# Kernel optimization log

Measured on AMD Instinct MI355X. Metric: run time of the kernel, lower is better.

## Reference

```python
import jax, jax.numpy as jnp
import numpy as np

N = 50000   # nodes
E = 800000  # directed edges
D = 128     # input_channels


def _kaiming(key, shape):
    fan_in = shape[0]
    return jax.random.normal(key, shape, jnp.float32) * np.float32(np.sqrt(2.0 / fan_in))


def setup_inputs():
    key = jax.random.key(0)
    ks = jax.random.split(key, 8)
    x = jax.random.normal(ks[0], (N, D), jnp.float32)
    edge_index = jax.random.randint(ks[1], (2, E), 0, N, dtype=jnp.int32)
    return {
        "x": x,
        "edge_index": edge_index,
        "W_in": _kaiming(ks[2], (D, D)),      "b_in": jnp.zeros((D,), jnp.float32),
        "W1": _kaiming(ks[3], (D, 2 * D)),    "b1": jnp.zeros((2 * D,), jnp.float32),
        "W2": _kaiming(ks[4], (2 * D, D)),    "b2": jnp.zeros((D,), jnp.float32),
        "W3": _kaiming(ks[5], (D, D // 2)),   "b3": jnp.zeros((D // 2,), jnp.float32),
        "W_out": _kaiming(ks[6], (D // 2, 1)), "b_out": jnp.zeros((1,), jnp.float32),
    }


def _gcn_conv(x, src, dst, W, b, n):
    """PyG GCNConv: add self-loops, symmetric D^-1/2 (A+I) D^-1/2 normalization."""
    h = x @ W  # [n, out]
    loop = jnp.arange(n, dtype=src.dtype)
    s = jnp.concatenate([src, loop])  # message sources (x_j)
    d = jnp.concatenate([dst, loop])  # aggregation targets (x_i)
    deg = jax.ops.segment_sum(jnp.ones_like(d, jnp.float32), d, num_segments=n)
    dis = jnp.where(deg > 0, jax.lax.rsqrt(jnp.maximum(deg, 1.0)), 0.0)
    norm = dis[s] * dis[d]  # [E+n]
    msg = h[s] * norm[:, None]  # gather + scale
    out = jax.ops.segment_sum(msg, d, num_segments=n)  # scatter-add
    return out + b


def reference(x, edge_index, W_in, b_in, W1, b1, W2, b2, W3, b3, W_out, b_out):
    src, dst = edge_index[0], edge_index[1]
    n = x.shape[0]
    lrelu = lambda t: jax.nn.leaky_relu(t, 0.01)
    # dropout in eval mode (identity)
    h = lrelu(x @ W_in + b_in)
    h = lrelu(_gcn_conv(h, src, dst, W1, b1, n))
    h = lrelu(_gcn_conv(h, src, dst, W2, b2, n))
    h = lrelu(_gcn_conv(h, src, dst, W3, b3, n))
    return h @ W_out + b_out  # [n, 1]
```

## Files before the change

### kernel.cpp

```cpp
#include <hip/hip_runtime.h>
#include <hip/hip_cooperative_groups.h>

namespace cg = cooperative_groups;


#define LRELU(v) ((v) > 0.f ? (v) : 0.01f * (v))

typedef __attribute__((ext_vector_type(8))) _Float16 half8;
typedef __attribute__((ext_vector_type(8))) float float8;
typedef __attribute__((ext_vector_type(4))) float floatx4;

constexpr int CAP = 64;
constexpr int SMEM_H = 16896;

template <int K, int F, int EPI, typename IT>
__device__ void phase_gemm(const IT* __restrict__ X,
                           const _Float16* __restrict__ Wt,
                           const float* __restrict__ b,
                           const int* __restrict__ cnt,
                           _Float16* __restrict__ out, int M,
                           _Float16* xs) {
  constexpr int TM = 64;
  constexpr int LK = K + 8;
  constexpr int CW = F / 4;
  constexpr int NT = CW / 16;
  constexpr int NK = K / 32;

  const int tid = threadIdx.x;
  const int w = tid >> 6;
  const int lane = tid & 63;
  const int m = lane & 15;
  const int q = lane >> 4;
  const int nTiles = (M + TM - 1) / TM;

  half8 breg[NT][NK];
#pragma unroll
  for (int t = 0; t < NT; ++t)
#pragma unroll
    for (int kc = 0; kc < NK; ++kc)
      breg[t][kc] =
          *(const half8*)&Wt[(long)(w * CW + t * 16 + m) * K + kc * 32 + q * 8];

  for (int tile = blockIdx.x; tile < nTiles; tile += gridDim.x) {
    const int m0 = tile * TM;
    __syncthreads();
    constexpr int CPR = K / 8;
    for (int idx = tid; idx < TM * CPR; idx += 256) {
      const int row = idx / CPR;
      const int kk = idx % CPR;
      const int g = m0 + row;
      half8 h = (half8)(_Float16)0.f;
      if (g < M) {
        if constexpr (sizeof(IT) == 4) {
          const float4* p = (const float4*)&X[(long)g * K + kk * 8];
          float4 a = p[0], c = p[1];
          h[0] = (_Float16)a.x; h[1] = (_Float16)a.y;
          h[2] = (_Float16)a.z; h[3] = (_Float16)a.w;
          h[4] = (_Float16)c.x; h[5] = (_Float16)c.y;
          h[6] = (_Float16)c.z; h[7] = (_Float16)c.w;
        } else {
          h = *(const half8*)&X[(long)g * K + kk * 8];
        }
      }
      *(half8*)&xs[row * LK + kk * 8] = h;
    }
    __syncthreads();

    floatx4 acc[4][NT];
#pragma unroll
    for (int rt = 0; rt < 4; ++rt)
#pragma unroll
      for (int t = 0; t < NT; ++t) acc[rt][t] = (floatx4){0.f, 0.f, 0.f, 0.f};

#pragma unroll
    for (int kc = 0; kc < NK; ++kc) {
      half8 af[4];
#pragma unroll
      for (int rt = 0; rt < 4; ++rt)
        af[rt] = *(const half8*)&xs[(rt * 16 + m) * LK + kc * 32 + q * 8];
#pragma unroll
      for (int rt = 0; rt < 4; ++rt)
#pragma unroll
        for (int t = 0; t < NT; ++t)
          acc[rt][t] = __builtin_amdgcn_mfma_f32_16x16x32_f16(
              af[rt], breg[t][kc], acc[rt][t], 0, 0, 0);
    }

#pragma unroll
    for (int rt = 0; rt < 4; ++rt) {
#pragma unroll
      for (int r = 0; r < 4; ++r) {
        const int row = m0 + rt * 16 + q * 4 + r;
        if (row < M) {
          const float dv = rsqrtf((float)cnt[row] + 1.0f);
#pragma unroll
          for (int t = 0; t < NT; ++t) {
            const int col = w * CW + t * 16 + m;
            float v = acc[rt][t][r];
            if constexpr (EPI == 0) { v += b[col]; v = LRELU(v); v *= dv; }
            if constexpr (EPI == 2) { v *= dv; }
            out[(long)row * F + col] = (_Float16)v;
          }
        }
      }
    }
  }
}

__device__ void phase_gemm2x(const _Float16* __restrict__ X,
                             const _Float16* __restrict__ Wt1,
                             const float* __restrict__ b1,
                             const _Float16* __restrict__ Wt2,
                             const int* __restrict__ cnt,
                             _Float16* __restrict__ out, int M,
                             _Float16* smem) {
  constexpr int TM = 64;
  constexpr int LK1 = 128 + 8;
  constexpr int LK2 = 256 + 8;
  _Float16* xs = smem;
  _Float16* ys = smem;

  const int tid = threadIdx.x;
  const int w = tid >> 6;
  const int lane = tid & 63;
  const int m = lane & 15;
  const int q = lane >> 4;
  const int nTiles = (M + TM - 1) / TM;

  half8 breg1[4][4];
#pragma unroll
  for (int t = 0; t < 4; ++t)
#pragma unroll
    for (int kc = 0; kc < 4; ++kc)
      breg1[t][kc] = *(const half8*)&Wt1[(long)(w * 64 + t * 16 + m) * 128 +
                                         kc * 32 + q * 8];
  half8 breg2[2][8];
#pragma unroll
  for (int t = 0; t < 2; ++t)
#pragma unroll
    for (int kc = 0; kc < 8; ++kc)
      breg2[t][kc] = *(const half8*)&Wt2[(long)(w * 32 + t * 16 + m) * 256 +
                                         kc * 32 + q * 8];

  for (int tile = blockIdx.x; tile < nTiles; tile += gridDim.x) {
    const int m0 = tile * TM;
    __syncthreads();
    for (int idx = tid; idx < TM * 16; idx += 256) {
      const int row = idx >> 4;
      const int kk = idx & 15;
      const int g = m0 + row;
      half8 h = (half8)(_Float16)0.f;
      if (g < M) h = *(const half8*)&X[(long)g * 128 + kk * 8];
      *(half8*)&xs[row * LK1 + kk * 8] = h;
    }
    __syncthreads();

    floatx4 acc1[4][4];
#pragma unroll
    for (int rt = 0; rt < 4; ++rt)
#pragma unroll
      for (int t = 0; t < 4; ++t) acc1[rt][t] = (floatx4){0.f, 0.f, 0.f, 0.f};

#pragma unroll
    for (int kc = 0; kc < 4; ++kc) {
      half8 af[4];
#pragma unroll
      for (int rt = 0; rt < 4; ++rt)
        af[rt] = *(const half8*)&xs[(rt * 16 + m) * LK1 + kc * 32 + q * 8];
#pragma unroll
      for (int rt = 0; rt < 4; ++rt)
#pragma unroll
        for (int t = 0; t < 4; ++t)
          acc1[rt][t] = __builtin_amdgcn_mfma_f32_16x16x32_f16(
              af[rt], breg1[t][kc], acc1[rt][t], 0, 0, 0);
    }
    __syncthreads();

#pragma unroll
    for (int rt = 0; rt < 4; ++rt) {
#pragma unroll
      for (int r = 0; r < 4; ++r) {
        const int row = rt * 16 + q * 4 + r;
#pragma unroll
        for (int t = 0; t < 4; ++t) {
          const int col = w * 64 + t * 16 + m;
          float v = acc1[rt][t][r] + b1[col];
          ys[row * LK2 + col] = (_Float16)LRELU(v);
        }
      }
    }
    __syncthreads();

    floatx4 acc2[4][2];
#pragma unroll
    for (int rt = 0; rt < 4; ++rt)
#pragma unroll
      for (int t = 0; t < 2; ++t) acc2[rt][t] = (floatx4){0.f, 0.f, 0.f, 0.f};

#pragma unroll
    for (int kc = 0; kc < 8; ++kc) {
      half8 af[4];
#pragma unroll
      for (int rt = 0; rt < 4; ++rt)
        af[rt] = *(const half8*)&ys[(rt * 16 + m) * LK2 + kc * 32 + q * 8];
#pragma unroll
      for (int rt = 0; rt < 4; ++rt)
#pragma unroll
        for (int t = 0; t < 2; ++t)
          acc2[rt][t] = __builtin_amdgcn_mfma_f32_16x16x32_f16(
              af[rt], breg2[t][kc], acc2[rt][t], 0, 0, 0);
    }

#pragma unroll
    for (int rt = 0; rt < 4; ++rt) {
#pragma unroll
      for (int r = 0; r < 4; ++r) {
        const int row = m0 + rt * 16 + q * 4 + r;
        if (row < M) {
          const float dv = rsqrtf((float)cnt[row] + 1.0f);
#pragma unroll
          for (int t = 0; t < 2; ++t) {
            const int col = w * 32 + t * 16 + m;
            out[(long)row * 128 + col] = (_Float16)(acc2[rt][t][r] * dv);
          }
        }
      }
    }
  }
}

template <int F, int MODE>
__device__ void phase_agg(const _Float16* __restrict__ G,
                          const unsigned short* __restrict__ pad,
                          const int* __restrict__ cnt,
                          const float* __restrict__ b,
                          const float* __restrict__ Wout,
                          const float* __restrict__ bout,
                          void* __restrict__ out, int N) {
  const int w = threadIdx.x >> 6;
  const int lane = threadIdx.x & 63;
  const int c = lane & 7;
  const int j = lane >> 3;
  const int n = j >> 2;
  const int jj = j & 3;
  const int uBlk = (N + 7) / 8;
  const int nUnits = (F == 128) ? 2 * uBlk : uBlk;

  for (int u = blockIdx.x; u < nUnits; u += gridDim.x) {
    const int y = (F == 128) ? (u / uBlk) : 0;
    const int ub = (F == 128) ? (u % uBlk) : u;
    int i = ub * 8 + w * 2 + n;
    const bool valid = (i < N);
    if (!valid) i = N - 1;
    const int col0 = y << 6;

    const _Float16* gbase = G + col0 + c * 8;
    const int cn = min(cnt[i], CAP);
    const unsigned short* plist = pad + (long)i * CAP;

    float8 acc = {0.f, 0.f, 0.f, 0.f, 0.f, 0.f, 0.f, 0.f};
    if (jj == 0)
      acc = __builtin_convertvector(*(const half8*)(gbase + (long)i * F), float8);
    for (int e = jj; e < cn; e += 4) {
      const int s = plist[e];
      acc += __builtin_convertvector(*(const half8*)(gbase + (long)s * F), float8);
    }
#pragma unroll
    for (int k = 0; k < 8; ++k) {
      acc[k] += __shfl_xor(acc[k], 8);
      acc[k] += __shfl_xor(acc[k], 16);
    }

    const float dv = rsqrtf((float)cnt[i] + 1.0f);
    if constexpr (MODE == 2) {
      float p = 0.f;
#pragma unroll
      for (int k = 0; k < 8; ++k) {
        const int col = c * 8 + k;
        float v = acc[k] * dv + b[col];
        v = LRELU(v);
        p += v * Wout[col];
      }
      p += __shfl_xor(p, 1);
      p += __shfl_xor(p, 2);
      p += __shfl_xor(p, 4);
      if (valid && jj == 0 && c == 0) ((float*)out)[i] = p + bout[0];
    } else {
      if (valid && jj == 0) {
        half8 hv;
#pragma unroll
        for (int k = 0; k < 8; ++k) {
          float v = acc[k] * dv;
          if constexpr (MODE == 1) { v += b[col0 + c * 8 + k]; v = LRELU(v); }
          hv[k] = (_Float16)v;
        }
        *(half8*)&((_Float16*)out)[(long)i * F + col0 + c * 8] = hv;
      }
    }
  }
}

__global__ __launch_bounds__(256, 2) void k_mega(
    const float* __restrict__ x, const int* __restrict__ src,
    const int* __restrict__ dst, const float* __restrict__ W_in,
    const float* __restrict__ b_in, const float* __restrict__ W1,
    const float* __restrict__ b1, const float* __restrict__ W2,
    const float* __restrict__ b2, const float* __restrict__ W3,
    const float* __restrict__ b3, const float* __restrict__ W_out,
    const float* __restrict__ b_out, int* __restrict__ cnt,
    unsigned short* __restrict__ pad, _Float16* __restrict__ wt_in,
    _Float16* __restrict__ wt1, _Float16* __restrict__ wt2,
    _Float16* __restrict__ wt3, _Float16* __restrict__ buf1,
    _Float16* __restrict__ buf2, _Float16* __restrict__ buf3,
    float* __restrict__ out, int N, int E, int PR) {
  cg::grid_group grid = cg::this_grid();
  __shared__ _Float16 smem[SMEM_H];

  const int tid = threadIdx.x;
  const int b = blockIdx.x;
  const int gid = b * 256 + tid;
  const int GS = gridDim.x * 256;

  for (int i = gid; i < N; i += GS) cnt[i] = 0;
  for (int i = gid; i < 128 * 128; i += GS) {
    const int k = i >> 7, f = i & 127;
    wt_in[f * 128 + k] = (_Float16)W_in[i];
  }
  for (int i = gid; i < 128 * 256; i += GS) {
    const int k = i >> 8, f = i & 255;
    wt1[f * 128 + k] = (_Float16)W1[i];
  }
  for (int i = gid; i < 256 * 128; i += GS) {
    const int k = i >> 7, f = i & 127;
    wt2[f * 256 + k] = (_Float16)W2[i];
  }
  for (int i = gid; i < 128 * 64; i += GS) {
    const int k = i >> 6, f = i & 63;
    wt3[f * 128 + k] = (_Float16)W3[i];
  }
  grid.sync();

  {
    const int range = b & 7;
    const int stride = (gridDim.x >> 3) * 256;
    for (int e = (b >> 3) * 256 + tid; e < E; e += stride) {
      const int d = dst[e];
      if (d / PR == range) {
        const int pos = atomicAdd(&cnt[d], 1);
        if (pos < CAP) pad[(long)d * CAP + pos] = (unsigned short)src[e];
      }
    }
  }
  grid.sync();

  phase_gemm<128, 128, 0, float>(x, wt_in, b_in, cnt, buf1, N, smem);
  grid.sync();
  phase_agg<128, 0>(buf1, pad, cnt, nullptr, nullptr, nullptr, buf2, N);
  grid.sync();
  phase_gemm2x(buf2, wt1, b1, wt2, cnt, buf1, N, smem);
  grid.sync();
  phase_agg<128, 1>(buf1, pad, cnt, b2, nullptr, nullptr, buf2, N);
  grid.sync();
  phase_gemm<128, 64, 2, _Float16>(buf2, wt3, nullptr, cnt, buf3, N, smem);
  grid.sync();
  phase_agg<64, 2>(buf3, pad, cnt, b3, W_out, b_out, out, N);
}

__global__ __launch_bounds__(256) void k_prep(const int* __restrict__ src,
                                              const int* __restrict__ dst,
                                              int* __restrict__ cnt,
                                              unsigned short* __restrict__ pad,
                                              const float* __restrict__ W_in,
                                              const float* __restrict__ W1,
                                              const float* __restrict__ W2,
                                              const float* __restrict__ W3,
                                              _Float16* __restrict__ wt_in,
                                              _Float16* __restrict__ wt1,
                                              _Float16* __restrict__ wt2,
                                              _Float16* __restrict__ wt3,
                                              int E, int PR) {
  const int b = blockIdx.x;
  const int tid = threadIdx.x;
  if (b < 128) {
    const int m = b >> 5;
    const int idx = (b & 31) * 256 + tid;
    if (m == 0) {
      for (int i = idx; i < 128 * 128; i += 8192) {
        const int k = i >> 7, f = i & 127;
        wt_in[f * 128 + k] = (_Float16)W_in[i];
      }
    } else if (m == 1) {
      for (int i = idx; i < 128 * 256; i += 8192) {
        const int k = i >> 8, f = i & 255;
        wt1[f * 128 + k] = (_Float16)W1[i];
      }
    } else if (m == 2) {
      for (int i = idx; i < 256 * 128; i += 8192) {
        const int k = i >> 7, f = i & 127;
        wt2[f * 256 + k] = (_Float16)W2[i];
      }
    } else {
      for (int i = idx; i < 128 * 64; i += 8192) {
        const int k = i >> 6, f = i & 63;
        wt3[f * 128 + k] = (_Float16)W3[i];
      }
    }
  } else {
    const int bb = b - 128;
    const int range = bb & 7;
    const int e = (bb >> 3) * 256 + tid;
    if (e < E) {
      const int d = dst[e];
      if (d / PR == range) {
        const int pos = atomicAdd(&cnt[d], 1);
        if (pos < CAP) pad[(long)d * CAP + pos] = (unsigned short)src[e];
      }
    }
  }
}

template <int K, int F, int EPI, typename IT>
__global__ __launch_bounds__(256) void k_gemm(const IT* __restrict__ X,
                                              const _Float16* __restrict__ Wt,
                                              const float* __restrict__ b,
                                              const int* __restrict__ cnt,
                                              _Float16* __restrict__ out, int M) {
  __shared__ _Float16 smem[64 * (K + 8)];
  phase_gemm<K, F, EPI, IT>(X, Wt, b, cnt, out, M, smem);
}

__global__ __launch_bounds__(256) void k_gemm2x(const _Float16* __restrict__ X,
                                                const _Float16* __restrict__ Wt1,
                                                const float* __restrict__ b1,
                                                const _Float16* __restrict__ Wt2,
                                                const int* __restrict__ cnt,
                                                _Float16* __restrict__ out,
                                                int M) {
  __shared__ _Float16 smem[SMEM_H];
  phase_gemm2x(X, Wt1, b1, Wt2, cnt, out, M, smem);
}

template <int F, int MODE>
__global__ __launch_bounds__(256) void k_agg(const _Float16* __restrict__ G,
                                             const unsigned short* __restrict__ pad,
                                             const int* __restrict__ cnt,
                                             const float* __restrict__ b,
                                             const float* __restrict__ Wout,
                                             const float* __restrict__ bout,
                                             void* __restrict__ out, int N) {
  phase_agg<F, MODE>(G, pad, cnt, b, Wout, bout, out, N);
}


extern "C" void kernel_launch(void* const* d_in, const int* in_sizes, int n_in,
                              void* d_out, int out_size, void* d_ws, size_t ws_size,
                              hipStream_t stream) {
  const float* x     = (const float*)d_in[0];
  const int* eidx    = (const int*)d_in[1];
  const float* W_in  = (const float*)d_in[2];
  const float* b_in  = (const float*)d_in[3];
  const float* W1    = (const float*)d_in[4];
  const float* b1    = (const float*)d_in[5];
  const float* W2    = (const float*)d_in[6];
  const float* b2    = (const float*)d_in[7];
  const float* W3    = (const float*)d_in[8];
  const float* b3    = (const float*)d_in[9];
  const float* W_out = (const float*)d_in[10];
  const float* b_out = (const float*)d_in[11];
  float* out = (float*)d_out;

  int N = in_sizes[0] / 128;
  int E = in_sizes[1] / 2;
  const int* src = eidx;
  const int* dst = eidx + E;
  int PR = (N + 7) / 8;

  size_t off = 0;
  char* base = (char*)d_ws;
  auto alloc = [&](size_t bytes) -> void* {
    void* p = base + off;
    off = (off + bytes + 255) & ~(size_t)255;
    return p;
  };
  int* cnt            = (int*)alloc((size_t)N * sizeof(int));
  unsigned short* pad = (unsigned short*)alloc((size_t)N * CAP * 2);
  _Float16* wt_in     = (_Float16*)alloc((size_t)128 * 128 * 2);
  _Float16* wt1       = (_Float16*)alloc((size_t)256 * 128 * 2);
  _Float16* wt2       = (_Float16*)alloc((size_t)128 * 256 * 2);
  _Float16* wt3       = (_Float16*)alloc((size_t)64 * 128 * 2);
  _Float16* buf1      = (_Float16*)alloc((size_t)N * 128 * 2);
  _Float16* buf2      = (_Float16*)alloc((size_t)N * 128 * 2);
  _Float16* buf3      = (_Float16*)alloc((size_t)N * 64 * 2);

  int dev = 0;
  hipGetDevice(&dev);
  int numCU = 0;
  hipDeviceGetAttribute(&numCU, hipDeviceAttributeMultiprocessorCount, dev);
  int maxB = 0;
  hipError_t qe = hipOccupancyMaxActiveBlocksPerMultiprocessor(
      &maxB, (const void*)k_mega, 256, 0);
  int grid = (qe == hipSuccess && numCU > 0) ? maxB * numCU : 0;
  grid &= ~7;
  if (grid > 2048) grid = 2048;

  bool coop = (grid >= 8);
  if (coop) {
    void* kargs[] = {
        (void*)&x,     (void*)&src,  (void*)&dst,  (void*)&W_in,
        (void*)&b_in,  (void*)&W1,   (void*)&b1,   (void*)&W2,
        (void*)&b2,    (void*)&W3,   (void*)&b3,   (void*)&W_out,
        (void*)&b_out, (void*)&cnt,  (void*)&pad,  (void*)&wt_in,
        (void*)&wt1,   (void*)&wt2,  (void*)&wt3,  (void*)&buf1,
        (void*)&buf2,  (void*)&buf3, (void*)&out,  (void*)&N,
        (void*)&E,     (void*)&PR};
    hipError_t le = hipLaunchCooperativeKernel((const void*)k_mega, dim3(grid),
                                               dim3(256), kargs, 0, stream);
    coop = (le == hipSuccess);
  }

  if (!coop) {
    const int gE = (E + 255) / 256;
    const int gRows = (N + 63) / 64;
    const int gAggP = (N + 7) / 8;
    hipMemsetAsync(cnt, 0, (size_t)N * sizeof(int), stream);
    k_prep<<<128 + 8 * gE, 256, 0, stream>>>(src, dst, cnt, pad, W_in, W1, W2,
                                             W3, wt_in, wt1, wt2, wt3, E, PR);
    k_gemm<128, 128, 0, float><<<gRows, 256, 0, stream>>>(x, wt_in, b_in, cnt,
                                                          buf1, N);
    k_agg<128, 0><<<2 * gAggP, 256, 0, stream>>>(buf1, pad, cnt, nullptr,
                                                 nullptr, nullptr, buf2, N);
    k_gemm2x<<<gRows, 256, 0, stream>>>(buf2, wt1, b1, wt2, cnt, buf1, N);
    k_agg<128, 1><<<2 * gAggP, 256, 0, stream>>>(buf1, pad, cnt, b2, nullptr,
                                                 nullptr, buf2, N);
    k_gemm<128, 64, 2, _Float16><<<gRows, 256, 0, stream>>>(buf2, wt3, nullptr,
                                                            cnt, buf3, N);
    k_agg<64, 2><<<gAggP, 256, 0, stream>>>(buf3, pad, cnt, b3, W_out, b_out,
                                            out, N);
  }
}
```

Measured before the change: 327.1 us.

## Split fused double GEMM and stream weights per tile to raise occupancy

Replaces the fused gemm2x phase (128→256→128 with an intermediate kept in shared memory) with two separate GEMM phases that go through a new N×256 fp16 global buffer. The per-phase weight fragments are no longer held in registers for the whole kernel; they are reloaded per column group and K chunk inside the tile loop. Launch bounds rise from 2 to 4 blocks per CU to cut register pressure and allow a larger cooperative grid. In exchange it adds an extra grid.sync, global traffic for the 256-wide intermediate, and repeated weight loads from cache on every tile.

```diff
diff --git a/kernel.cpp b/kernel.cpp
--- a/kernel.cpp
+++ b/kernel.cpp
@@ -13,7 +13,7 @@
 constexpr int CAP = 64;
 constexpr int SMEM_H = 16896;
 
-template <int K, int F, int EPI, typename IT>
+template <int K, int F, int EPI, int CG, int KG, typename IT>
 __device__ void phase_gemm(const IT* __restrict__ X,
                            const _Float16* __restrict__ Wt,
                            const float* __restrict__ b,
@@ -23,8 +23,10 @@
   constexpr int TM = 64;
   constexpr int LK = K + 8;
   constexpr int CW = F / 4;
-  constexpr int NT = CW / 16;
-  constexpr int NK = K / 32;
+  constexpr int CPW = CW / CG;
+  constexpr int NT = CPW / 16;
+  constexpr int KH = K / KG;
+  constexpr int NKg = KH / 32;
 
   const int tid = threadIdx.x;
   const int w = tid >> 6;
@@ -32,14 +34,6 @@
   const int m = lane & 15;
   const int q = lane >> 4;
   const int nTiles = (M + TM - 1) / TM;
-
-  half8 breg[NT][NK];
-#pragma unroll
-  for (int t = 0; t < NT; ++t)
-#pragma unroll
-    for (int kc = 0; kc < NK; ++kc)
-      breg[t][kc] =
-          *(const half8*)&Wt[(long)(w * CW + t * 16 + m) * K + kc * 32 + q * 8];
 
   for (int tile = blockIdx.x; tile < nTiles; tile += gridDim.x) {
     const int m0 = tile * TM;
@@ -66,162 +60,54 @@
     }
     __syncthreads();
 
-    floatx4 acc[4][NT];
-#pragma unroll
-    for (int rt = 0; rt < 4; ++rt)
-#pragma unroll
-      for (int t = 0; t < NT; ++t) acc[rt][t] = (floatx4){0.f, 0.f, 0.f, 0.f};
-
-#pragma unroll
-    for (int kc = 0; kc < NK; ++kc) {
-      half8 af[4];
+    for (int cg = 0; cg < CG; ++cg) {
+      const int colbase = w * CW + cg * CPW;
+      floatx4 acc[4][NT];
 #pragma unroll
       for (int rt = 0; rt < 4; ++rt)
-        af[rt] = *(const half8*)&xs[(rt * 16 + m) * LK + kc * 32 + q * 8];
-#pragma unroll
-      for (int rt = 0; rt < 4; ++rt)
+#pragma unroll
+        for (int t = 0; t < NT; ++t) acc[rt][t] = (floatx4){0.f, 0.f, 0.f, 0.f};
+
+      for (int kg = 0; kg < KG; ++kg) {
+        half8 breg[NT][NKg];
 #pragma unroll
         for (int t = 0; t < NT; ++t)
-          acc[rt][t] = __builtin_amdgcn_mfma_f32_16x16x32_f16(
-              af[rt], breg[t][kc], acc[rt][t], 0, 0, 0);
-    }
-
-#pragma unroll
-    for (int rt = 0; rt < 4; ++rt) {
-#pragma unroll
-      for (int r = 0; r < 4; ++r) {
-        const int row = m0 + rt * 16 + q * 4 + r;
-        if (row < M) {
-          const float dv = rsqrtf((float)cnt[row] + 1.0f);
-#pragma unroll
-          for (int t = 0; t < NT; ++t) {
-            const int col = w * CW + t * 16 + m;
-            float v = acc[rt][t][r];
-            if constexpr (EPI == 0) { v += b[col]; v = LRELU(v); v *= dv; }
-            if constexpr (EPI == 2) { v *= dv; }
-            out[(long)row * F + col] = (_Float16)v;
-          }
+#pragma unroll
+          for (int kc = 0; kc < NKg; ++kc)
+            breg[t][kc] = *(const half8*)&Wt[(long)(colbase + t * 16 + m) * K +
+                                             kg * KH + kc * 32 + q * 8];
+#pragma unroll
+        for (int kc = 0; kc < NKg; ++kc) {
+          half8 af[4];
+#pragma unroll
+          for (int rt = 0; rt < 4; ++rt)
+            af[rt] = *(const half8*)&xs[(rt * 16 + m) * LK + kg * KH + kc * 32 +
+                                        q * 8];
+#pragma unroll
+          for (int rt = 0; rt < 4; ++rt)
+#pragma unroll
+            for (int t = 0; t < NT; ++t)
+              acc[rt][t] = __builtin_amdgcn_mfma_f32_16x16x32_f16(
+                  af[rt], breg[t][kc], acc[rt][t], 0, 0, 0);
         }
       }
-    }
-  }
-}
-
-__device__ void phase_gemm2x(const _Float16* __restrict__ X,
-                             const _Float16* __restrict__ Wt1,
-                             const float* __restrict__ b1,
-                             const _Float16* __restrict__ Wt2,
-                             const int* __restrict__ cnt,
-                             _Float16* __restrict__ out, int M,
-                             _Float16* smem) {
-  constexpr int TM = 64;
-  constexpr int LK1 = 128 + 8;
-  constexpr int LK2 = 256 + 8;
-  _Float16* xs = smem;
-  _Float16* ys = smem;
-
-  const int tid = threadIdx.x;
-  const int w = tid >> 6;
-  const int lane = tid & 63;
-  const int m = lane & 15;
-  const int q = lane >> 4;
-  const int nTiles = (M + TM - 1) / TM;
-
-  half8 breg1[4][4];
-#pragma unroll
-  for (int t = 0; t < 4; ++t)
-#pragma unroll
-    for (int kc = 0; kc < 4; ++kc)
-      breg1[t][kc] = *(const half8*)&Wt1[(long)(w * 64 + t * 16 + m) * 128 +
-                                         kc * 32 + q * 8];
-  half8 breg2[2][8];
-#pragma unroll
-  for (int t = 0; t < 2; ++t)
-#pragma unroll
-    for (int kc = 0; kc < 8; ++kc)
-      breg2[t][kc] = *(const half8*)&Wt2[(long)(w * 32 + t * 16 + m) * 256 +
-                                         kc * 32 + q * 8];
-
-  for (int tile = blockIdx.x; tile < nTiles; tile += gridDim.x) {
-    const int m0 = tile * TM;
-    __syncthreads();
-    for (int idx = tid; idx < TM * 16; idx += 256) {
-      const int row = idx >> 4;
-      const int kk = idx & 15;
-      const int g = m0 + row;
-      half8 h = (half8)(_Float16)0.f;
-      if (g < M) h = *(const half8*)&X[(long)g * 128 + kk * 8];
-      *(half8*)&xs[row * LK1 + kk * 8] = h;
-    }
-    __syncthreads();
-
-    floatx4 acc1[4][4];
-#pragma unroll
-    for (int rt = 0; rt < 4; ++rt)
-#pragma unroll
-      for (int t = 0; t < 4; ++t) acc1[rt][t] = (floatx4){0.f, 0.f, 0.f, 0.f};
-
-#pragma unroll
-    for (int kc = 0; kc < 4; ++kc) {
-      half8 af[4];
-#pragma unroll
-      for (int rt = 0; rt < 4; ++rt)
-        af[rt] = *(const half8*)&xs[(rt * 16 + m) * LK1 + kc * 32 + q * 8];
-#pragma unroll
-      for (int rt = 0; rt < 4; ++rt)
-#pragma unroll
-        for (int t = 0; t < 4; ++t)
-          acc1[rt][t] = __builtin_amdgcn_mfma_f32_16x16x32_f16(
-              af[rt], breg1[t][kc], acc1[rt][t], 0, 0, 0);
-    }
-    __syncthreads();
-
-#pragma unroll
-    for (int rt = 0; rt < 4; ++rt) {
-#pragma unroll
-      for (int r = 0; r < 4; ++r) {
-        const int row = rt * 16 + q * 4 + r;
-#pragma unroll
-        for (int t = 0; t < 4; ++t) {
-          const int col = w * 64 + t * 16 + m;
-          float v = acc1[rt][t][r] + b1[col];
-          ys[row * LK2 + col] = (_Float16)LRELU(v);
-        }
-      }
-    }
-    __syncthreads();
-
-    floatx4 acc2[4][2];
-#pragma unroll
-    for (int rt = 0; rt < 4; ++rt)
-#pragma unroll
-      for (int t = 0; t < 2; ++t) acc2[rt][t] = (floatx4){0.f, 0.f, 0.f, 0.f};
-
-#pragma unroll
-    for (int kc = 0; kc < 8; ++kc) {
-      half8 af[4];
-#pragma unroll
-      for (int rt = 0; rt < 4; ++rt)
-        af[rt] = *(const half8*)&ys[(rt * 16 + m) * LK2 + kc * 32 + q * 8];
-#pragma unroll
-      for (int rt = 0; rt < 4; ++rt)
-#pragma unroll
-        for (int t = 0; t < 2; ++t)
-          acc2[rt][t] = __builtin_amdgcn_mfma_f32_16x16x32_f16(
-              af[rt], breg2[t][kc], acc2[rt][t], 0, 0, 0);
-    }
-
-#pragma unroll
-    for (int rt = 0; rt < 4; ++rt) {
-#pragma unroll
-      for (int r = 0; r < 4; ++r) {
-        const int row = m0 + rt * 16 + q * 4 + r;
-        if (row < M) {
-          const float dv = rsqrtf((float)cnt[row] + 1.0f);
-#pragma unroll
-          for (int t = 0; t < 2; ++t) {
-            const int col = w * 32 + t * 16 + m;
-            out[(long)row * 128 + col] = (_Float16)(acc2[rt][t][r] * dv);
+
+#pragma unroll
+      for (int rt = 0; rt < 4; ++rt) {
+#pragma unroll
+        for (int r = 0; r < 4; ++r) {
+          const int row = m0 + rt * 16 + q * 4 + r;
+          if (row < M) {
+            const float dv = rsqrtf((float)cnt[row] + 1.0f);
+#pragma unroll
+            for (int t = 0; t < NT; ++t) {
+              const int col = colbase + t * 16 + m;
+              float v = acc[rt][t][r];
+              if constexpr (EPI == 0) { v += b[col]; v = LRELU(v); v *= dv; }
+              if constexpr (EPI == 1) { v += b[col]; v = LRELU(v); }
+              if constexpr (EPI == 2) { v *= dv; }
+              out[(long)row * F + col] = (_Float16)v;
+            }
           }
         }
       }
@@ -300,7 +186,7 @@
   }
 }
 
-__global__ __launch_bounds__(256, 2) void k_mega(
+__global__ __launch_bounds__(256, 4) void k_mega(
     const float* __restrict__ x, const int* __restrict__ src,
     const int* __restrict__ dst, const float* __restrict__ W_in,
     const float* __restrict__ b_in, const float* __restrict__ W1,
@@ -312,7 +198,8 @@
     _Float16* __restrict__ wt1, _Float16* __restrict__ wt2,
     _Float16* __restrict__ wt3, _Float16* __restrict__ buf1,
     _Float16* __restrict__ buf2, _Float16* __restrict__ buf3,
-    float* __restrict__ out, int N, int E, int PR) {
+    _Float16* __restrict__ bufg3, float* __restrict__ out,
+    int N, int E, int PR) {
   cg::grid_group grid = cg::this_grid();
   __shared__ _Float16 smem[SMEM_H];
 
@@ -353,17 +240,19 @@
   }
   grid.sync();
 
-  phase_gemm<128, 128, 0, float>(x, wt_in, b_in, cnt, buf1, N, smem);
+  phase_gemm<128, 128, 0, 1, 1, float>(x, wt_in, b_in, cnt, buf1, N, smem);
   grid.sync();
   phase_agg<128, 0>(buf1, pad, cnt, nullptr, nullptr, nullptr, buf2, N);
   grid.sync();
-  phase_gemm2x(buf2, wt1, b1, wt2, cnt, buf1, N, smem);
+  phase_gemm<128, 256, 1, 2, 1, _Float16>(buf2, wt1, b1, cnt, buf3, N, smem);
+  grid.sync();
+  phase_gemm<256, 128, 2, 1, 2, _Float16>(buf3, wt2, nullptr, cnt, buf1, N, smem);
   grid.sync();
   phase_agg<128, 1>(buf1, pad, cnt, b2, nullptr, nullptr, buf2, N);
   grid.sync();
-  phase_gemm<128, 64, 2, _Float16>(buf2, wt3, nullptr, cnt, buf3, N, smem);
-  grid.sync();
-  phase_agg<64, 2>(buf3, pad, cnt, b3, W_out, b_out, out, N);
+  phase_gemm<128, 64, 2, 1, 1, _Float16>(buf2, wt3, nullptr, cnt, bufg3, N, smem);
+  grid.sync();
+  phase_agg<64, 2>(bufg3, pad, cnt, b3, W_out, b_out, out, N);
 }
 
 __global__ __launch_bounds__(256) void k_prep(const int* __restrict__ src,
@@ -419,25 +308,14 @@
   }
 }
 
-template <int K, int F, int EPI, typename IT>
+template <int K, int F, int EPI, int CG, int KG, typename IT>
 __global__ __launch_bounds__(256) void k_gemm(const IT* __restrict__ X,
                                               const _Float16* __restrict__ Wt,
                                               const float* __restrict__ b,
                                               const int* __restrict__ cnt,
                                               _Float16* __restrict__ out, int M) {
   __shared__ _Float16 smem[64 * (K + 8)];
-  phase_gemm<K, F, EPI, IT>(X, Wt, b, cnt, out, M, smem);
-}
-
-__global__ __launch_bounds__(256) void k_gemm2x(const _Float16* __restrict__ X,
-                                                const _Float16* __restrict__ Wt1,
-                                                const float* __restrict__ b1,
-                                                const _Float16* __restrict__ Wt2,
-                                                const int* __restrict__ cnt,
-                                                _Float16* __restrict__ out,
-                                                int M) {
-  __shared__ _Float16 smem[SMEM_H];
-  phase_gemm2x(X, Wt1, b1, Wt2, cnt, out, M, smem);
+  phase_gemm<K, F, EPI, CG, KG, IT>(X, Wt, b, cnt, out, M, smem);
 }
 
 template <int F, int MODE>
@@ -490,7 +368,8 @@
   _Float16* wt3       = (_Float16*)alloc((size_t)64 * 128 * 2);
   _Float16* buf1      = (_Float16*)alloc((size_t)N * 128 * 2);
   _Float16* buf2      = (_Float16*)alloc((size_t)N * 128 * 2);
-  _Float16* buf3      = (_Float16*)alloc((size_t)N * 64 * 2);
+  _Float16* buf3      = (_Float16*)alloc((size_t)N * 256 * 2);
+  _Float16* bufg3     = (_Float16*)alloc((size_t)N * 64 * 2);
 
   int dev = 0;
   hipGetDevice(&dev);
@@ -506,13 +385,13 @@
   bool coop = (grid >= 8);
   if (coop) {
     void* kargs[] = {
-        (void*)&x,     (void*)&src,  (void*)&dst,  (void*)&W_in,
-        (void*)&b_in,  (void*)&W1,   (void*)&b1,   (void*)&W2,
-        (void*)&b2,    (void*)&W3,   (void*)&b3,   (void*)&W_out,
-        (void*)&b_out, (void*)&cnt,  (void*)&pad,  (void*)&wt_in,
-        (void*)&wt1,   (void*)&wt2,  (void*)&wt3,  (void*)&buf1,
-        (void*)&buf2,  (void*)&buf3, (void*)&out,  (void*)&N,
-        (void*)&E,     (void*)&PR};
+        (void*)&x,     (void*)&src,  (void*)&dst,   (void*)&W_in,
+        (void*)&b_in,  (void*)&W1,   (void*)&b1,    (void*)&W2,
+        (void*)&b2,    (void*)&W3,   (void*)&b3,    (void*)&W_out,
+        (void*)&b_out, (void*)&cnt,  (void*)&pad,   (void*)&wt_in,
+        (void*)&wt1,   (void*)&wt2,  (void*)&wt3,   (void*)&buf1,
+        (void*)&buf2,  (void*)&buf3, (void*)&bufg3, (void*)&out,
+        (void*)&N,     (void*)&E,    (void*)&PR};
     hipError_t le = hipLaunchCooperativeKernel((const void*)k_mega, dim3(grid),
                                                dim3(256), kargs, 0, stream);
     coop = (le == hipSuccess);
@@ -525,16 +404,19 @@
     hipMemsetAsync(cnt, 0, (size_t)N * sizeof(int), stream);
     k_prep<<<128 + 8 * gE, 256, 0, stream>>>(src, dst, cnt, pad, W_in, W1, W2,
                                              W3, wt_in, wt1, wt2, wt3, E, PR);
-    k_gemm<128, 128, 0, float><<<gRows, 256, 0, stream>>>(x, wt_in, b_in, cnt,
-                                                          buf1, N);
+    k_gemm<128, 128, 0, 1, 1, float><<<gRows, 256, 0, stream>>>(
+        x, wt_in, b_in, cnt, buf1, N);
     k_agg<128, 0><<<2 * gAggP, 256, 0, stream>>>(buf1, pad, cnt, nullptr,
                                                  nullptr, nullptr, buf2, N);
-    k_gemm2x<<<gRows, 256, 0, stream>>>(buf2, wt1, b1, wt2, cnt, buf1, N);
+    k_gemm<128, 256, 1, 2, 1, _Float16><<<gRows, 256, 0, stream>>>(
+        buf2, wt1, b1, cnt, buf3, N);
+    k_gemm<256, 128, 2, 1, 2, _Float16><<<gRows, 256, 0, stream>>>(
+        buf3, wt2, nullptr, cnt, buf1, N);
     k_agg<128, 1><<<2 * gAggP, 256, 0, stream>>>(buf1, pad, cnt, b2, nullptr,
                                                  nullptr, buf2, N);
-    k_gemm<128, 64, 2, _Float16><<<gRows, 256, 0, stream>>>(buf2, wt3, nullptr,
-                                                            cnt, buf3, N);
-    k_agg<64, 2><<<gAggP, 256, 0, stream>>>(buf3, pad, cnt, b3, W_out, b_out,
+    k_gemm<128, 64, 2, 1, 1, _Float16><<<gRows, 256, 0, stream>>>(
+        buf2, wt3, nullptr, cnt, bufg3, N);
+    k_agg<64, 2><<<gAggP, 256, 0, stream>>>(bufg3, pad, cnt, b3, W_out, b_out,
                                             out, N);
   }
 }
```

Result: no change. 332.1 us (+1.5%).
